# Kernel tuning notes

Hardware: AMD Instinct MI355X
Metric: run time of the kernel (lower is better)

## Reference

```python
import jax, jax.numpy as jnp
import numpy as np

SQRT_DK = np.sqrt(512.0).astype(np.float32)


def setup_inputs() -> dict:
    key = jax.random.key(0)
    k1, k2, k3 = jax.random.split(key, 3)
    x = jax.random.normal(k1, (16, 2048, 512), dtype=jnp.float32)
    W1 = jax.random.normal(k2, (512, 10), dtype=jnp.float32) * 0.05
    W2 = jax.random.normal(k3, (10, 512), dtype=jnp.float32) * 0.05
    return {"x": x, "W1": W1, "W2": W2}


def reference(x, W1, W2):
    # x: [B, A, D]; low-rank bilinear scores: (x@W1) @ (W2@x^T) -> [B, A, A]
    B, A, D = x.shape
    left = jnp.einsum('bad,dr->bar', x, W1)          # [B, A, 10]
    right = jnp.einsum('rd,bcd->brc', W2, x)         # [B, 10, A]
    scores = jnp.einsum('bar,brc->bac', left, right)  # [B, A, A]
    attn = jax.nn.softmax(scores / SQRT_DK, axis=-1)
    out = jnp.einsum('bac,bcd->bad', attn, x)         # requires_value=True
    return out
```

## Files before the change

### kernel.cpp

```cpp
#include <hip/hip_runtime.h>
#include <cstdint>
#include <cstddef>


typedef float    f32x4 __attribute__((ext_vector_type(4)));
typedef _Float16 half8 __attribute__((ext_vector_type(8)));
typedef _Float16 half4 __attribute__((ext_vector_type(4)));
typedef _Float16 half2 __attribute__((ext_vector_type(2)));

#define B_  16
#define A_  2048
#define D_  512
#define KSCALE 0.06375872f

__device__ inline float fast_exp2(float v) {
#if __has_builtin(__builtin_amdgcn_exp2f)
    return __builtin_amdgcn_exp2f(v);
#else
    return __expf(v * 0.6931471805599453f);
#endif
}

__global__ __launch_bounds__(256) void kw_prep(const float* __restrict__ W1,
                                               const float* __restrict__ W2,
                                               _Float16* __restrict__ Wf) {
    int pi = blockIdx.x * 256 + threadIdx.x;
    int kt = pi >> 6, lane = pi & 63;
    int quad = lane >> 4, col = lane & 15;
    half8 h1, h2;
#pragma unroll
    for (int j = 0; j < 8; ++j) {
        int d = kt * 32 + quad * 8 + j;
        h1[j] = (col < 10) ? (_Float16)(W1[d * 10 + col] * KSCALE) : (_Float16)0.f;
        h2[j] = (col < 10) ? (_Float16)W2[col * 512 + d] : (_Float16)0.f;
    }
    *(half8*)(Wf + (size_t)pi * 16) = h1;
    *(half8*)(Wf + (size_t)pi * 16 + 8) = h2;
}

__global__ __launch_bounds__(256) void k01_prep(const float* __restrict__ x,
                                                const _Float16* __restrict__ Wf,
                                                _Float16* __restrict__ xT,
                                                _Float16* __restrict__ left16,
                                                _Float16* __restrict__ rightT16) {
    __shared__ float xs[32 * 64];
    int t = threadIdx.x, lane = t & 63, w = t >> 6;
    int quad = lane >> 4, c16 = lane & 15;
    int bid = blockIdx.x;
    int b = bid >> 6, grp = bid & 63;
    int c0 = grp << 5;
    const float* xb = x + ((size_t)b * A_ + c0) * D_;
    int tile = w >> 1, kki = w & 1;
    int ar = tile * 16 + c16;
    f32x4 accA = {0.f, 0.f, 0.f, 0.f}, accB = {0.f, 0.f, 0.f, 0.f};

    for (int dc = 0; dc < 8; ++dc) {
        __syncthreads();
#pragma unroll
        for (int p = 0; p < 2; ++p) {
            int c = p * 16 + (t >> 4), ch = t & 15;
            float4 v = *(const float4*)(xb + (size_t)c * D_ + dc * 64 + ch * 4);
            *(float4*)&xs[c * 64 + ((ch ^ (c & 15)) << 2)] = v;
        }
        __syncthreads();
        {
            int dloc = t >> 2, c8 = (t & 3) << 3;
            int ch = dloc >> 2, e = dloc & 3;
            half8 h;
#pragma unroll
            for (int j = 0; j < 8; ++j) {
                int c = c8 + j;
                h[j] = (_Float16)xs[c * 64 + ((ch ^ (c & 15)) << 2) + e];
            }
            *(half8*)(xT + ((size_t)b * D_ + dc * 64 + dloc) * A_ + c0 + c8) = h;
        }
        {
            int kk = kki * 32;
            int ch0 = (kk >> 2) + quad * 2;
            float4 v0 = *(const float4*)&xs[ar * 64 + ((ch0 ^ c16) << 2)];
            float4 v1 = *(const float4*)&xs[ar * 64 + (((ch0 + 1) ^ c16) << 2)];
            half8 af;
            af[0] = (_Float16)v0.x; af[1] = (_Float16)v0.y; af[2] = (_Float16)v0.z; af[3] = (_Float16)v0.w;
            af[4] = (_Float16)v1.x; af[5] = (_Float16)v1.y; af[6] = (_Float16)v1.z; af[7] = (_Float16)v1.w;
            const half8* wf = (const half8*)(Wf + ((size_t)((dc * 2 + kki) * 64 + lane)) * 16);
            half8 b1 = wf[0], b2 = wf[1];
            accA = __builtin_amdgcn_mfma_f32_16x16x32_f16(af, b1, accA, 0, 0, 0);
            accB = __builtin_amdgcn_mfma_f32_16x16x32_f16(af, b2, accB, 0, 0, 0);
        }
    }
    __syncthreads();
    float* red = xs;
    if (kki == 0) {
#pragma unroll
        for (int q = 0; q < 4; ++q) {
            red[tile * 512 + (quad * 4 + q) * 16 + c16] = accA[q];
            red[tile * 512 + 256 + (quad * 4 + q) * 16 + c16] = accB[q];
        }
    }
    __syncthreads();
    if (kki == 1) {
#pragma unroll
        for (int q = 0; q < 4; ++q) {
            float a = accA[q] + red[tile * 512 + (quad * 4 + q) * 16 + c16];
            float bb = accB[q] + red[tile * 512 + 256 + (quad * 4 + q) * 16 + c16];
            size_t grow = (size_t)bid * 32 + tile * 16 + quad * 4 + q;
            left16[grow * 16 + c16] = (_Float16)a;
            rightT16[grow * 16 + c16] = (_Float16)bb;
        }
    }
}

__global__ __launch_bounds__(256, 3) void k3_attn(const _Float16* __restrict__ xT,
                                                  const _Float16* __restrict__ left16,
                                                  const _Float16* __restrict__ rightT16,
                                                  float* __restrict__ out) {
    __shared__ _Float16 XTl[2][128 * 32];
    __shared__ _Float16 Ps[2][128 * 40];
    __shared__ float rowsum[128];
    int t = threadIdx.x, lane = t & 63, w = t >> 6;
    int quad = lane >> 4, c16 = lane & 15;
    int bid = blockIdx.x;
    int combo = (bid & 7) | (((bid >> 7) & 7) << 3);
    int at = (bid >> 3) & 15;
    int b = combo >> 2, nb = combo & 3;
    int a0 = at << 7, n0 = nb << 7;
    int waveM = w & 1, waveN = w >> 1;

    half8 lf8[2];
#pragma unroll
    for (int i = 0; i < 2; ++i) {
        lf8[i] = (half8)(_Float16)0.f;
        if (quad < 2) {
            int arow = a0 + (2 * w + i) * 16 + c16;
            lf8[i] = *(const half8*)(left16 + ((size_t)(b << 11) + arow) * 16 + quad * 8);
        }
    }

    f32x4 acc[4][4];
#pragma unroll
    for (int mi = 0; mi < 4; ++mi)
#pragma unroll
        for (int ni = 0; ni < 4; ++ni) acc[mi][ni] = (f32x4){0.f, 0.f, 0.f, 0.f};
    float psum[2] = {0.f, 0.f};

    const _Float16* xTb = xT + ((size_t)b * D_ + n0) * A_;
    const _Float16* rTb = rightT16 + (size_t)(b << 11) * 16;

    int nloc0 = w * 32 + (lane >> 2);
    int kq = lane & 3;

    auto dma_tile = [&](int kt, int buf) {
        int c0 = kt << 5;
#pragma unroll
        for (int cc = 0; cc < 2; ++cc) {
            int nl = nloc0 + cc * 16;
            int kqs = kq ^ ((nl >> 1) & 3);
            const _Float16* src = xTb + (size_t)nl * A_ + c0 + kqs * 8;
            _Float16* dst = &XTl[buf][(w * 32 + cc * 16) * 32];
            __builtin_amdgcn_global_load_lds((const __attribute__((address_space(1))) void*)src,
                                             (__attribute__((address_space(3))) void*)dst,
                                             16, 0, 0);
        }
    };
    auto load_bfr = [&](int kt, half8* bfr) {
#pragma unroll
        for (int nh = 0; nh < 2; ++nh) {
            bfr[nh] = (half8)(_Float16)0.f;
            if (quad < 2) {
                int crow = (kt << 5) + nh * 16 + c16;
                bfr[nh] = *(const half8*)(rTb + (size_t)crow * 16 + quad * 8);
            }
        }
    };
    auto p_phase = [&](const half8* bfr, int buf) {
#pragma unroll
        for (int nh = 0; nh < 2; ++nh) {
#pragma unroll
            for (int i = 0; i < 2; ++i) {
                f32x4 z = {0.f, 0.f, 0.f, 0.f};
                f32x4 pc = __builtin_amdgcn_mfma_f32_16x16x32_f16(bfr[nh], lf8[i], z, 0, 0, 0);
                float e0 = fast_exp2(pc[0]), e1 = fast_exp2(pc[1]);
                float e2 = fast_exp2(pc[2]), e3 = fast_exp2(pc[3]);
                psum[i] += (e0 + e1) + (e2 + e3);
                half4 pv;
                pv[0] = (_Float16)e0; pv[1] = (_Float16)e1;
                pv[2] = (_Float16)e2; pv[3] = (_Float16)e3;
                *(half4*)&Ps[buf][((2 * w + i) * 16 + c16) * 40 + nh * 16 + quad * 4] = pv;
            }
        }
    };

    {
        half8 bfr0[2];
        dma_tile(0, 0);
        load_bfr(0, bfr0);
        p_phase(bfr0, 0);
    }

    for (int kt = 0; kt < 64; ++kt) {
        __syncthreads();
        int cb = kt & 1, nxt = kt + 1;
        half8 bfr[2];
        if (nxt < 64) {
            dma_tile(nxt, nxt & 1);
            load_bfr(nxt, bfr);
        }
        half8 af[4], bf[4];
#pragma unroll
        for (int mi = 0; mi < 4; ++mi)
            af[mi] = *(const half8*)&Ps[cb][(waveM * 64 + mi * 16 + c16) * 40 + quad * 8];
#pragma unroll
        for (int ni = 0; ni < 4; ++ni) {
            int nr = waveN * 64 + ni * 16 + c16;
            bf[ni] = *(const half8*)&XTl[cb][nr * 32 + ((quad ^ ((nr >> 1) & 3)) << 3)];
        }
#pragma unroll
        for (int mi = 0; mi < 4; ++mi)
#pragma unroll
            for (int ni = 0; ni < 4; ++ni)
                acc[mi][ni] = __builtin_amdgcn_mfma_f32_16x16x32_f16(af[mi], bf[ni], acc[mi][ni], 0, 0, 0);
        if (nxt < 64) p_phase(bfr, nxt & 1);
    }

#pragma unroll
    for (int i = 0; i < 2; ++i) {
        float s = psum[i];
        s += __shfl_xor(s, 16);
        s += __shfl_xor(s, 32);
        if (quad == 0) rowsum[(2 * w + i) * 16 + c16] = s;
    }
    __syncthreads();

    float* ob = out + ((size_t)b * A_ + a0) * D_ + n0;
#pragma unroll
    for (int mi = 0; mi < 4; ++mi) {
#pragma unroll
        for (int q = 0; q < 4; ++q) {
            int ar = waveM * 64 + mi * 16 + quad * 4 + q;
            float sc = 1.0f / rowsum[ar];
#pragma unroll
            for (int ni = 0; ni < 4; ++ni)
                ob[(size_t)ar * D_ + waveN * 64 + ni * 16 + c16] = acc[mi][ni][q] * sc;
        }
    }
}

extern "C" void kernel_launch(void* const* d_in, const int* in_sizes, int n_in,
                              void* d_out, int out_size, void* d_ws, size_t ws_size,
                              hipStream_t stream) {
    const float* x  = (const float*)d_in[0];
    const float* W1 = (const float*)d_in[1];
    const float* W2 = (const float*)d_in[2];
    float* out = (float*)d_out;
    char* ws = (char*)d_ws;
    _Float16* xT      = (_Float16*)ws;
    _Float16* left16  = (_Float16*)(ws + 33554432);
    _Float16* rightT16= (_Float16*)(ws + 34603008);
    _Float16* Wf      = (_Float16*)(ws + 35651584);

    kw_prep<<<4, 256, 0, stream>>>(W1, W2, Wf);
    k01_prep<<<1024, 256, 0, stream>>>(x, Wf, xT, left16, rightT16);
    k3_attn<<<1024, 256, 0, stream>>>(xT, left16, rightT16, out);
}
```

Before: 230.3 us.

## Split prep into async-LDS transpose kernel and register-direct factor GEMM kernel

Replaces the fused prep kernel, which staged x through shared memory behind eight rounds of barriers, with two kernels. One transposes x to fp16 using global_load_lds direct-to-LDS loads over a larger 128x64 tile with one barrier. The other computes the low-rank left/right factors straight from global memory into MFMA without LDS or a cross-wave reduction. The cost is reading x twice (once per kernel) plus an extra launch, traded for more parallelism and fewer synchronisations.

```diff
diff --git a/kernel.cpp b/kernel.cpp
--- a/kernel.cpp
+++ b/kernel.cpp
@@ -38,75 +38,67 @@
     *(half8*)(Wf + (size_t)pi * 16 + 8) = h2;
 }
 
-__global__ __launch_bounds__(256) void k01_prep(const float* __restrict__ x,
-                                                const _Float16* __restrict__ Wf,
-                                                _Float16* __restrict__ xT,
-                                                _Float16* __restrict__ left16,
-                                                _Float16* __restrict__ rightT16) {
-    __shared__ float xs[32 * 64];
+__global__ __launch_bounds__(256) void kt_transpose(const float* __restrict__ x,
+                                                    _Float16* __restrict__ xT) {
+    __shared__ float xs[128 * 64];
+    int t = threadIdx.x, w = t >> 6;
+    int bid = blockIdx.x;
+    int b = bid >> 7, cg = (bid >> 3) & 15, dg = bid & 7;
+    int c0 = cg << 7, d0 = dg << 6;
+    const float* xb = x + ((size_t)(b * A_ + c0)) * D_ + d0;
+#pragma unroll
+    for (int it = 0; it < 8; ++it) {
+        int slot = it * 256 + t;
+        int c = slot >> 4, g = slot & 15;
+        int gs = g ^ (c >> 3);
+        const float* src = xb + (size_t)c * D_ + (gs << 2);
+        float* dst = xs + (size_t)(it * 256 + w * 64) * 4;
+        __builtin_amdgcn_global_load_lds((const __attribute__((address_space(1))) void*)src,
+                                         (__attribute__((address_space(3))) void*)dst,
+                                         16, 0, 0);
+    }
+    __syncthreads();
+    _Float16* xTb = xT + ((size_t)b * D_ + d0) * A_ + c0;
+#pragma unroll
+    for (int p = 0; p < 4; ++p) {
+        int dloc = p * 16 + (t >> 4);
+        int c8 = (t & 15) << 3;
+        int gd = dloc >> 2, e = dloc & 3;
+        half8 h;
+#pragma unroll
+        for (int j = 0; j < 8; ++j) {
+            int c = c8 + j;
+            h[j] = (_Float16)xs[c * 64 + ((gd ^ (c >> 3)) << 2) + e];
+        }
+        *(half8*)(xTb + (size_t)dloc * A_ + c8) = h;
+    }
+}
+
+__global__ __launch_bounds__(256) void kf_factors(const float* __restrict__ x,
+                                                  const _Float16* __restrict__ Wf,
+                                                  _Float16* __restrict__ left16,
+                                                  _Float16* __restrict__ rightT16) {
     int t = threadIdx.x, lane = t & 63, w = t >> 6;
     int quad = lane >> 4, c16 = lane & 15;
-    int bid = blockIdx.x;
-    int b = bid >> 6, grp = bid & 63;
-    int c0 = grp << 5;
-    const float* xb = x + ((size_t)b * A_ + c0) * D_;
-    int tile = w >> 1, kki = w & 1;
-    int ar = tile * 16 + c16;
+    size_t arow0 = (size_t)blockIdx.x * 64 + (size_t)w * 16;
+    const float* xa = x + (arow0 + c16) * D_;
     f32x4 accA = {0.f, 0.f, 0.f, 0.f}, accB = {0.f, 0.f, 0.f, 0.f};
-
-    for (int dc = 0; dc < 8; ++dc) {
-        __syncthreads();
-#pragma unroll
-        for (int p = 0; p < 2; ++p) {
-            int c = p * 16 + (t >> 4), ch = t & 15;
-            float4 v = *(const float4*)(xb + (size_t)c * D_ + dc * 64 + ch * 4);
-            *(float4*)&xs[c * 64 + ((ch ^ (c & 15)) << 2)] = v;
-        }
-        __syncthreads();
-        {
-            int dloc = t >> 2, c8 = (t & 3) << 3;
-            int ch = dloc >> 2, e = dloc & 3;
-            half8 h;
-#pragma unroll
-            for (int j = 0; j < 8; ++j) {
-                int c = c8 + j;
-                h[j] = (_Float16)xs[c * 64 + ((ch ^ (c & 15)) << 2) + e];
-            }
-            *(half8*)(xT + ((size_t)b * D_ + dc * 64 + dloc) * A_ + c0 + c8) = h;
-        }
-        {
-            int kk = kki * 32;
-            int ch0 = (kk >> 2) + quad * 2;
-            float4 v0 = *(const float4*)&xs[ar * 64 + ((ch0 ^ c16) << 2)];
-            float4 v1 = *(const float4*)&xs[ar * 64 + (((ch0 + 1) ^ c16) << 2)];
-            half8 af;
-            af[0] = (_Float16)v0.x; af[1] = (_Float16)v0.y; af[2] = (_Float16)v0.z; af[3] = (_Float16)v0.w;
-            af[4] = (_Float16)v1.x; af[5] = (_Float16)v1.y; af[6] = (_Float16)v1.z; af[7] = (_Float16)v1.w;
-            const half8* wf = (const half8*)(Wf + ((size_t)((dc * 2 + kki) * 64 + lane)) * 16);
-            half8 b1 = wf[0], b2 = wf[1];
-            accA = __builtin_amdgcn_mfma_f32_16x16x32_f16(af, b1, accA, 0, 0, 0);
-            accB = __builtin_amdgcn_mfma_f32_16x16x32_f16(af, b2, accB, 0, 0, 0);
-        }
-    }
-    __syncthreads();
-    float* red = xs;
-    if (kki == 0) {
-#pragma unroll
-        for (int q = 0; q < 4; ++q) {
-            red[tile * 512 + (quad * 4 + q) * 16 + c16] = accA[q];
-            red[tile * 512 + 256 + (quad * 4 + q) * 16 + c16] = accB[q];
-        }
-    }
-    __syncthreads();
-    if (kki == 1) {
-#pragma unroll
-        for (int q = 0; q < 4; ++q) {
-            float a = accA[q] + red[tile * 512 + (quad * 4 + q) * 16 + c16];
-            float bb = accB[q] + red[tile * 512 + 256 + (quad * 4 + q) * 16 + c16];
-            size_t grow = (size_t)bid * 32 + tile * 16 + quad * 4 + q;
-            left16[grow * 16 + c16] = (_Float16)a;
-            rightT16[grow * 16 + c16] = (_Float16)bb;
-        }
+#pragma unroll
+    for (int kc = 0; kc < 16; ++kc) {
+        float4 v0 = *(const float4*)(xa + kc * 32 + quad * 8);
+        float4 v1 = *(const float4*)(xa + kc * 32 + quad * 8 + 4);
+        half8 af;
+        af[0] = (_Float16)v0.x; af[1] = (_Float16)v0.y; af[2] = (_Float16)v0.z; af[3] = (_Float16)v0.w;
+        af[4] = (_Float16)v1.x; af[5] = (_Float16)v1.y; af[6] = (_Float16)v1.z; af[7] = (_Float16)v1.w;
+        const half8* wf = (const half8*)(Wf + ((size_t)(kc * 64 + lane)) * 16);
+        accA = __builtin_amdgcn_mfma_f32_16x16x32_f16(af, wf[0], accA, 0, 0, 0);
+        accB = __builtin_amdgcn_mfma_f32_16x16x32_f16(af, wf[1], accB, 0, 0, 0);
+    }
+#pragma unroll
+    for (int q = 0; q < 4; ++q) {
+        size_t grow = arow0 + (size_t)quad * 4 + q;
+        left16[grow * 16 + c16]   = (_Float16)accA[q];
+        rightT16[grow * 16 + c16] = (_Float16)accB[q];
     }
 }
 
@@ -259,6 +251,7 @@
     _Float16* Wf      = (_Float16*)(ws + 35651584);
 
     kw_prep<<<4, 256, 0, stream>>>(W1, W2, Wf);
-    k01_prep<<<1024, 256, 0, stream>>>(x, Wf, xT, left16, rightT16);
+    kt_transpose<<<2048, 256, 0, stream>>>(x, xT);
+    kf_factors<<<512, 256, 0, stream>>>(x, Wf, left16, rightT16);
     k3_attn<<<1024, 256, 0, stream>>>(xT, left16, rightT16, out);
 }
```

Result: slower. 236.6 us (+2.7%).
